# Kernel optimization log

Hardware: AMD Instinct MI355X
Metric: run time of the kernel (lower is better)

The kernel has to match this reference:

```python
import jax, jax.numpy as jnp
import numpy as np

B, L, D_MODEL, D_STATE, D_HIDDEN = 4, 4096, 1024, 256, 4096
RMIN, RMAX, MAX_PHASE = 0.8, 0.95, 2.0 * np.pi


def setup_inputs() -> dict:
    key = jax.random.key(0)
    ks = jax.random.split(key, 10)
    # LRU ring init (Orvieto et al.): |lambda| in [rmin, rmax], phase in [0, max_phase)
    u1 = jax.random.uniform(ks[0], (D_STATE,))
    u2 = jax.random.uniform(ks[1], (D_STATE,))
    nu_log = jnp.log(-0.5 * jnp.log(u1 * (RMAX**2 - RMIN**2) + RMIN**2))
    theta_log = jnp.log(MAX_PHASE * u2)
    B_re = jax.random.normal(ks[2], (D_STATE, D_MODEL)) / np.sqrt(2.0 * D_MODEL)
    B_im = jax.random.normal(ks[3], (D_STATE, D_MODEL)) / np.sqrt(2.0 * D_MODEL)
    C_re = jax.random.normal(ks[4], (D_MODEL, D_STATE)) / np.sqrt(D_STATE)
    C_im = jax.random.normal(ks[5], (D_MODEL, D_STATE)) / np.sqrt(D_STATE)
    D_mat = jax.random.normal(ks[6], (D_MODEL, D_MODEL)) / np.sqrt(D_MODEL)
    W1 = jax.random.normal(ks[7], (D_MODEL, D_HIDDEN)) * np.sqrt(2.0 / D_MODEL)
    W2 = jax.random.normal(ks[8], (D_HIDDEN, D_MODEL)) * np.sqrt(2.0 / D_HIDDEN)
    res_logit = jnp.asarray(-1.0, dtype=jnp.float32)
    x3d = jax.random.normal(ks[9], (B, L, D_MODEL), dtype=jnp.float32)
    return {"x3d": x3d, "nu_log": nu_log, "theta_log": theta_log,
            "B_re": B_re, "B_im": B_im, "C_re": C_re, "C_im": C_im,
            "D_mat": D_mat, "W1": W1, "W2": W2, "res_logit": res_logit}


def _lru_scan(lam, Bu):
    # diagonal linear recurrence x_t = lam * x_{t-1} + Bu_t via associative scan
    lam_b = jnp.broadcast_to(lam, Bu.shape)  # [B, L, N]

    def comb(a, b):
        return (a[0] * b[0], b[0] * a[1] + b[1])

    _, states = jax.lax.associative_scan(comb, (lam_b, Bu), axis=1)
    return states  # [B, L, N] complex


def reference(x3d, nu_log, theta_log, B_re, B_im, C_re, C_im, D_mat, W1, W2, res_logit):
    lam = jnp.exp(-jnp.exp(nu_log) + 1j * jnp.exp(theta_log))          # [N]
    gamma = jnp.sqrt(1.0 - jnp.abs(lam) ** 2)                           # [N]
    Bn = (gamma[:, None] * (B_re + 1j * B_im))                          # [N, D]
    Bu = jnp.einsum('bld,nd->bln', x3d.astype(jnp.complex64), Bn)       # [B, L, N]
    states = _lru_scan(lam.astype(jnp.complex64), Bu)                   # [B, L, N]
    y = jnp.einsum('bln,mn->blm', states, C_re + 1j * C_im).real \
        + jnp.einsum('bld,md->blm', x3d, D_mat)                         # [B, L, D]
    # MLP feedforward (nl_layers=2, bias=False), dropout is identity at p=0
    z = jax.nn.gelu(y @ W1) @ W2                                        # [B, L, D]
    out = x3d + jax.nn.sigmoid(res_logit) * z
    st = states[:, -1]  # final recurrent state
    return out, st
```

## Files before the change

kernel.cpp:

```cpp
#include <hip/hip_runtime.h>
#include <stdint.h>

typedef __bf16 bf16;
typedef bf16 bf16x8 __attribute__((ext_vector_type(8)));
typedef float f32x4 __attribute__((ext_vector_type(4)));

#define B_  4
#define L_  4096
#define DM  1024
#define DS  256
#define DH  4096
#define BL  16384
#define CL  64
#define NC  64

__device__ __forceinline__ float bfbits(uint32_t lo16) {
  union { uint32_t u; float f; } v; v.u = lo16 << 16; return v.f;
}

__device__ __forceinline__ void async16(const bf16* g, bf16* l) {
  __builtin_amdgcn_global_load_lds(
      (const __attribute__((address_space(1))) uint32_t*)g,
      (__attribute__((address_space(3))) uint32_t*)l, 16, 0, 0);
}

#define MEMFENCE() asm volatile("" ::: "memory")

__global__ void phaseA(const float* __restrict__ nu_log,
                       const float* __restrict__ th_log,
                       float* __restrict__ scal) {
  int n = threadIdx.x;
  float nu = __expf(nu_log[n]);
  float th = __expf(th_log[n]);
  float mod = __expf(-nu);
  float lr = mod * cosf(th);
  float li = mod * sinf(th);
  float g = sqrtf(fmaxf(1.0f - mod * mod, 0.0f));
  float pr = 1.f, pi = 0.f;
  for (int i = 0; i < CL; i++) {
    float nr = pr * lr - pi * li;
    float ni = pr * li + pi * lr;
    pr = nr; pi = ni;
  }
  scal[n] = lr; scal[256 + n] = li;
  scal[512 + n] = pr; scal[768 + n] = pi;
  scal[1024 + n] = g;
}

__global__ void prep_bu(const float* __restrict__ B_re, const float* __restrict__ B_im,
                        const float* __restrict__ scal, bf16* __restrict__ WB) {
  size_t i = (size_t)blockIdx.x * 256 + threadIdx.x;
  int row = (int)(i >> 10), col = (int)(i & 1023);
  int n = row >> 1;
  const float* src = (row & 1) ? B_im : B_re;
  WB[i] = (bf16)(scal[1024 + n] * src[n * 1024 + col]);
}

__global__ void prep_y(const float* __restrict__ C_re, const float* __restrict__ C_im,
                       const float* __restrict__ D_mat, bf16* __restrict__ WB) {
  size_t i = (size_t)blockIdx.x * 256 + threadIdx.x;
  int m = (int)(i / 1536), c = (int)(i % 1536);
  float v;
  if (c < 256)       v = C_re[m * 256 + c];
  else if (c < 512)  v = -C_im[m * 256 + (c - 256)];
  else               v = D_mat[m * 1024 + (c - 512)];
  WB[i] = (bf16)v;
}

__global__ void transpose_to_bf16(const float* __restrict__ in, bf16* __restrict__ out,
                                  int R, int C) {
  __shared__ float tile[32][33];
  int c0 = blockIdx.x * 32, r0 = blockIdx.y * 32;
  int tx = threadIdx.x, ty = threadIdx.y;
  for (int i = 0; i < 32; i += 8)
    tile[ty + i][tx] = in[(size_t)(r0 + ty + i) * C + c0 + tx];
  __syncthreads();
  for (int i = 0; i < 32; i += 8)
    out[(size_t)(c0 + ty + i) * R + r0 + tx] = (bf16)tile[tx][ty + i];
}

__global__ void conv_x(const float4* __restrict__ x, bf16* __restrict__ XS) {
  size_t i = (size_t)blockIdx.x * 256 + threadIdx.x;
  size_t t = i >> 8;
  int d4 = (int)(i & 255);
  float4 v = x[i];
  bf16* o = XS + t * 1536 + 512 + (size_t)d4 * 4;
  o[0] = (bf16)v.x; o[1] = (bf16)v.y; o[2] = (bf16)v.z; o[3] = (bf16)v.w;
}

template <int EPI>
__device__ __forceinline__ void epi_store(void* C, int ldc, size_t row, size_t col,
                                          float v, float sig, const float* xres) {
  size_t off = row * (size_t)ldc + col;
  if (EPI == 0) {
    ((bf16*)C)[off] = (bf16)v;
  } else if (EPI == 1) {
    float z = 0.7978845608f * (v + 0.044715f * v * v * v);
    float gv = v / (1.f + __expf(-2.f * z));
    ((bf16*)C)[off] = (bf16)gv;
  } else {
    ((float*)C)[off] = xres[off] + sig * v;
  }
}

template <int EPI>
__global__ __launch_bounds__(512, 2) void gemm256(
    const bf16* __restrict__ A, int lda,
    const bf16* __restrict__ Bt, int ldb,
    void* __restrict__ C, int ldc, int NK, int mt, int nt,
    const float* __restrict__ xres, const float* __restrict__ reslog) {
  __shared__ __align__(16) bf16 sA[2 * 16384];
  __shared__ __align__(16) bf16 sB[2 * 16384];

  const int tid  = threadIdx.x;
  const int lane = tid & 63;
  const int wave = tid >> 6;
  const int q = lane >> 4, l16 = lane & 15;
  const int wr = wave >> 2, wc = wave & 3;

  int nb = mt * nt;
  int per = nb >> 3;
  int t0 = (blockIdx.x & 7) * per + (blockIdx.x >> 3);
  int gsz = nt << 3;
  int g = t0 / gsz, r = t0 % gsz;
  size_t m0 = (size_t)(g * 8 + (r & 7)) * 256;
  size_t n0 = (size_t)(r >> 3) * 256;

  const int srow = tid >> 3;
  const int scol = (((tid & 7) ^ ((tid >> 3) & 7)) << 3);
  const bf16* gA = A  + (m0 + srow) * (size_t)lda + scol;
  const bf16* gB = Bt + (n0 + srow) * (size_t)ldb + scol;
  bf16* lA = sA + tid * 8;
  bf16* lB = sB + tid * 8;

  auto stageA = [&](int kt) {
    const bf16* s = gA + kt * 64;
    bf16* l = lA + (kt & 1) * 16384;
    async16(s, l);
    async16(s + (size_t)64  * lda, l + 4096);
    async16(s + (size_t)128 * lda, l + 8192);
    async16(s + (size_t)192 * lda, l + 12288);
  };
  auto stageB = [&](int kt) {
    const bf16* s = gB + kt * 64;
    bf16* l = lB + (kt & 1) * 16384;
    async16(s, l);
    async16(s + (size_t)64  * ldb, l + 4096);
    async16(s + (size_t)128 * ldb, l + 8192);
    async16(s + (size_t)192 * ldb, l + 12288);
  };

  stageA(0); stageB(0);
  __builtin_amdgcn_s_waitcnt(0x0F70);
  __builtin_amdgcn_s_barrier();
  MEMFENCE();

  const int sw  = (l16 & 7) << 3;
  const int qx0 = (q << 3) ^ sw;
  const int qx1 = ((q << 3) + 32) ^ sw;
  const bf16* Ard = sA + wr * 8192 + l16 * 64;
  const bf16* Brd = sB + (wc >> 1) * 8192 + ((wc & 1) * 64 + l16) * 64;

  f32x4 acc[8][4] = {};
  bf16x8 aL[4][2], aH[4][2], b[4][2];

  for (int t = 0; t < NK; ++t) {
    const int d = (t & 1) * 16384;
    const bf16* Ab = Ard + d;
    const bf16* Bb = Brd + d;

#pragma unroll
    for (int j = 0; j < 4; ++j) {
      aL[j][0] = *(const bf16x8*)&Ab[j * 1024 + qx0];
      aL[j][1] = *(const bf16x8*)&Ab[j * 1024 + qx1];
    }
#pragma unroll
    for (int n = 0; n < 4; ++n) {
      b[n][0] = *(const bf16x8*)&Bb[n * 1024 + qx0];
      b[n][1] = *(const bf16x8*)&Bb[n * 1024 + qx1];
    }
    if (t + 1 < NK) { stageA(t + 1); stageB(t + 1); }
    MEMFENCE();

    __builtin_amdgcn_s_setprio(1);
#pragma unroll
    for (int j = 0; j < 4; ++j)
#pragma unroll
      for (int n = 0; n < 4; ++n)
        acc[j][n] = __builtin_amdgcn_mfma_f32_16x16x32_bf16(aL[j][0], b[n][0], acc[j][n], 0, 0, 0);
#pragma unroll
    for (int j = 0; j < 4; ++j)
#pragma unroll
      for (int n = 0; n < 4; ++n)
        acc[j][n] = __builtin_amdgcn_mfma_f32_16x16x32_bf16(aL[j][1], b[n][1], acc[j][n], 0, 0, 0);

#pragma unroll
    for (int j = 0; j < 4; ++j) {
      aH[j][0] = *(const bf16x8*)&Ab[(4 + j) * 1024 + qx0];
      aH[j][1] = *(const bf16x8*)&Ab[(4 + j) * 1024 + qx1];
    }
#pragma unroll
    for (int j = 0; j < 4; ++j)
#pragma unroll
      for (int n = 0; n < 4; ++n)
        acc[4 + j][n] = __builtin_amdgcn_mfma_f32_16x16x32_bf16(aH[j][0], b[n][0], acc[4 + j][n], 0, 0, 0);
#pragma unroll
    for (int j = 0; j < 4; ++j)
#pragma unroll
      for (int n = 0; n < 4; ++n)
        acc[4 + j][n] = __builtin_amdgcn_mfma_f32_16x16x32_bf16(aH[j][1], b[n][1], acc[4 + j][n], 0, 0, 0);
    __builtin_amdgcn_s_setprio(0);

    MEMFENCE();
    __builtin_amdgcn_s_waitcnt(0x0F70);
    __builtin_amdgcn_s_barrier();
    MEMFENCE();
  }

  float sig = 0.f;
  if (EPI == 2) sig = 1.f / (1.f + __expf(-reslog[0]));
#pragma unroll
  for (int mi = 0; mi < 8; ++mi)
#pragma unroll
    for (int ni = 0; ni < 4; ++ni) {
      size_t col = n0 + wc * 64 + ni * 16 + l16;
#pragma unroll
      for (int r2 = 0; r2 < 4; ++r2) {
        size_t row = m0 + wr * 128 + mi * 16 + q * 4 + r2;
        epi_store<EPI>(C, ldc, row, col, acc[mi][ni][r2], sig, xres);
      }
    }
}

template <int EPI>
__global__ __launch_bounds__(512, 2) void gemm128(
    const bf16* __restrict__ A, int lda,
    const bf16* __restrict__ Bt, int ldb,
    void* __restrict__ C, int ldc, int NK, int mt, int nt,
    const float* __restrict__ xres, const float* __restrict__ reslog) {
  __shared__ __align__(16) bf16 sA[2 * 8192];
  __shared__ __align__(16) bf16 sB[2 * 16384];

  const int tid  = threadIdx.x;
  const int lane = tid & 63;
  const int wave = tid >> 6;
  const int q = lane >> 4, l16 = lane & 15;
  const int wr = wave >> 2, wc = wave & 3;

  int nb = mt * nt;
  int per = nb >> 3;
  int t0 = (blockIdx.x & 7) * per + (blockIdx.x >> 3);
  int gsz = nt << 3;
  int g = t0 / gsz, r = t0 % gsz;
  size_t m0 = (size_t)(g * 8 + (r & 7)) * 128;
  size_t n0 = (size_t)(r >> 3) * 256;

  const int srow = tid >> 3;
  const int scol = (((tid & 7) ^ ((tid >> 3) & 7)) << 3);
  const bf16* gA = A  + (m0 + srow) * (size_t)lda + scol;
  const bf16* gB = Bt + (n0 + srow) * (size_t)ldb + scol;
  bf16* lA = sA + tid * 8;
  bf16* lB = sB + tid * 8;

  auto stageA = [&](int kt) {
    const bf16* s = gA + kt * 64;
    bf16* l = lA + (kt & 1) * 8192;
    async16(s, l);
    async16(s + (size_t)64 * lda, l + 4096);
  };
  auto stageB = [&](int kt) {
    const bf16* s = gB + kt * 64;
    bf16* l = lB + (kt & 1) * 16384;
    async16(s, l);
    async16(s + (size_t)64  * ldb, l + 4096);
    async16(s + (size_t)128 * ldb, l + 8192);
    async16(s + (size_t)192 * ldb, l + 12288);
  };

  stageA(0); stageB(0);
  __builtin_amdgcn_s_waitcnt(0x0F70);
  __builtin_amdgcn_s_barrier();
  MEMFENCE();

  const int sw  = (l16 & 7) << 3;
  const int qx0 = (q << 3) ^ sw;
  const int qx1 = ((q << 3) + 32) ^ sw;
  const bf16* Ard = sA + (wr * 64 + l16) * 64;
  const bf16* Brd = sB + (wc >> 1) * 8192 + ((wc & 1) * 64 + l16) * 64;

  f32x4 acc[4][4] = {};
  bf16x8 a[4][2], b[4][2];

  for (int t = 0; t < NK; ++t) {
    const bf16* Ab = Ard + (t & 1) * 8192;
    const bf16* Bb = Brd + (t & 1) * 16384;

#pragma unroll
    for (int j = 0; j < 4; ++j) {
      a[j][0] = *(const bf16x8*)&Ab[j * 1024 + qx0];
      a[j][1] = *(const bf16x8*)&Ab[j * 1024 + qx1];
    }
#pragma unroll
    for (int n = 0; n < 4; ++n) {
      b[n][0] = *(const bf16x8*)&Bb[n * 1024 + qx0];
      b[n][1] = *(const bf16x8*)&Bb[n * 1024 + qx1];
    }
    if (t + 1 < NK) { stageA(t + 1); stageB(t + 1); }
    MEMFENCE();

    __builtin_amdgcn_s_setprio(1);
#pragma unroll
    for (int j = 0; j < 4; ++j)
#pragma unroll
      for (int n = 0; n < 4; ++n)
        acc[j][n] = __builtin_amdgcn_mfma_f32_16x16x32_bf16(a[j][0], b[n][0], acc[j][n], 0, 0, 0);
#pragma unroll
    for (int j = 0; j < 4; ++j)
#pragma unroll
      for (int n = 0; n < 4; ++n)
        acc[j][n] = __builtin_amdgcn_mfma_f32_16x16x32_bf16(a[j][1], b[n][1], acc[j][n], 0, 0, 0);
    __builtin_amdgcn_s_setprio(0);

    MEMFENCE();
    __builtin_amdgcn_s_waitcnt(0x0F70);
    __builtin_amdgcn_s_barrier();
    MEMFENCE();
  }

  float sig = 0.f;
  if (EPI == 2) sig = 1.f / (1.f + __expf(-reslog[0]));
#pragma unroll
  for (int mi = 0; mi < 4; ++mi)
#pragma unroll
    for (int ni = 0; ni < 4; ++ni) {
      size_t col = n0 + wc * 64 + ni * 16 + l16;
#pragma unroll
      for (int r2 = 0; r2 < 4; ++r2) {
        size_t row = m0 + wr * 64 + mi * 16 + q * 4 + r2;
        epi_store<EPI>(C, ldc, row, col, acc[mi][ni][r2], sig, xres);
      }
    }
}

__global__ void scan_pass1(const bf16* __restrict__ Bu, const float* __restrict__ scal,
                           float2* __restrict__ H) {
  int b = blockIdx.x >> 6, c = blockIdx.x & 63, n = threadIdx.x;
  float lr = scal[n], li = scal[256 + n];
  float sr = 0.f, si = 0.f;
  size_t t0 = (size_t)b * L_ + (size_t)c * CL;
  const uint32_t* p = (const uint32_t*)(Bu + t0 * 512) + n;
  for (int j = 0; j < CL; j++) {
    uint32_t u = p[(size_t)j * 256];
    float ur = bfbits(u & 0xffffu), ui = bfbits(u >> 16);
    float nr = lr * sr - li * si + ur;
    float ni = lr * si + li * sr + ui;
    sr = nr; si = ni;
  }
  H[(size_t)(b * NC + c) * 256 + n] = make_float2(sr, si);
}

__global__ void scan_pass2(const float2* __restrict__ H, const float* __restrict__ scal,
                           float2* __restrict__ Carry) {
  int b = blockIdx.x, n = threadIdx.x;
  float Pr = scal[512 + n], Pi = scal[768 + n];
  float cr = 0.f, ci = 0.f;
  for (int c = 0; c < NC; c++) {
    Carry[(size_t)(b * NC + c) * 256 + n] = make_float2(cr, ci);
    float2 h = H[(size_t)(b * NC + c) * 256 + n];
    float nr = Pr * cr - Pi * ci + h.x;
    float ni = Pr * ci + Pi * cr + h.y;
    cr = nr; ci = ni;
  }
}

__global__ void scan_pass3(const bf16* __restrict__ Bu, const float* __restrict__ scal,
                           const float2* __restrict__ Carry, bf16* __restrict__ XS,
                           float* __restrict__ st) {
  int b = blockIdx.x >> 6, c = blockIdx.x & 63, n = threadIdx.x;
  float lr = scal[n], li = scal[256 + n];
  float2 cv = Carry[(size_t)(b * NC + c) * 256 + n];
  float sr = cv.x, si = cv.y;
  size_t t0 = (size_t)b * L_ + (size_t)c * CL;
  const uint32_t* p = (const uint32_t*)(Bu + t0 * 512) + n;
  bf16* qp = XS + t0 * 1536 + n;
  for (int j = 0; j < CL; j++) {
    uint32_t u = p[(size_t)j * 256];
    float ur = bfbits(u & 0xffffu), ui = bfbits(u >> 16);
    float nr = lr * sr - li * si + ur;
    float ni = lr * si + li * sr + ui;
    sr = nr; si = ni;
    qp[(size_t)j * 1536] = (bf16)sr;
    qp[(size_t)j * 1536 + 256] = (bf16)si;
  }
  if (c == NC - 1) {
    st[(size_t)b * 256 + n] = sr;
    st[1024 + (size_t)b * 256 + n] = si;
  }
}

extern "C" void kernel_launch(void* const* d_in, const int* in_sizes, int n_in,
                              void* d_out, int out_size, void* d_ws, size_t ws_size,
                              hipStream_t stream) {
  const float* x      = (const float*)d_in[0];
  const float* nu_log = (const float*)d_in[1];
  const float* th_log = (const float*)d_in[2];
  const float* B_re   = (const float*)d_in[3];
  const float* B_im   = (const float*)d_in[4];
  const float* C_re   = (const float*)d_in[5];
  const float* C_im   = (const float*)d_in[6];
  const float* D_mat  = (const float*)d_in[7];
  const float* W1     = (const float*)d_in[8];
  const float* W2     = (const float*)d_in[9];
  const float* reslog = (const float*)d_in[10];

  char* wsb = (char*)d_ws;
  size_t off = 0;
  auto alloc = [&](size_t bytes) {
    void* p = wsb + off;
    off += (bytes + 255) & ~(size_t)255;
    return p;
  };
  float*  scal = (float*)alloc(5 * 256 * 4);
  bf16*   WBbu = (bf16*)alloc((size_t)512 * 1024 * 2);
  bf16*   WBy  = (bf16*)alloc((size_t)1024 * 1536 * 2);
  bf16*   WB1  = (bf16*)alloc((size_t)4096 * 1024 * 2);
  bf16*   WB2  = (bf16*)alloc((size_t)1024 * 4096 * 2);
  float2* H    = (float2*)alloc((size_t)B_ * NC * 256 * 8);
  float2* Cr   = (float2*)alloc((size_t)B_ * NC * 256 * 8);
  bf16*   Ybf  = (bf16*)alloc((size_t)BL * 1024 * 2);
  bf16*   XS   = (bf16*)alloc((size_t)BL * 1536 * 2);
  bf16*   Bu   = (bf16*)alloc((size_t)BL * 512 * 2);
  bf16*   Hbf  = XS;

  float* out = (float*)d_out;
  float* st  = out + (size_t)BL * DM;

  phaseA<<<1, 256, 0, stream>>>(nu_log, th_log, scal);
  prep_bu<<<512 * 1024 / 256, 256, 0, stream>>>(B_re, B_im, scal, WBbu);
  prep_y<<<1024 * 1536 / 256, 256, 0, stream>>>(C_re, C_im, D_mat, WBy);
  transpose_to_bf16<<<dim3(4096 / 32, 1024 / 32), dim3(32, 8), 0, stream>>>(W1, WB1, 1024, 4096);
  transpose_to_bf16<<<dim3(1024 / 32, 4096 / 32), dim3(32, 8), 0, stream>>>(W2, WB2, 4096, 1024);
  conv_x<<<BL * 256 / 256, 256, 0, stream>>>((const float4*)x, XS);

  gemm128<0><<<128 * 2, 512, 0, stream>>>(
      XS + 512, 1536, WBbu, 1024, Bu, 512, 16, 128, 2, nullptr, nullptr);

  scan_pass1<<<B_ * NC, 256, 0, stream>>>(Bu, scal, H);
  scan_pass2<<<B_, 256, 0, stream>>>(H, scal, Cr);
  scan_pass3<<<B_ * NC, 256, 0, stream>>>(Bu, scal, Cr, XS, st);

  gemm256<0><<<64 * 4, 512, 0, stream>>>(
      XS, 1536, WBy, 1536, Ybf, 1024, 24, 64, 4, nullptr, nullptr);

  for (int i = 0; i < 2; i++) {
    const bf16* Yc = Ybf + (size_t)i * 8192 * 1024;
    float* Oc = out + (size_t)i * 8192 * 1024;
    const float* Xc = x + (size_t)i * 8192 * 1024;
    gemm256<1><<<32 * 16, 512, 0, stream>>>(
        Yc, 1024, WB1, 1024, Hbf, 4096, 16, 32, 16, nullptr, nullptr);
    gemm128<2><<<64 * 4, 512, 0, stream>>>(
        Hbf, 4096, WB2, 4096, Oc, 1024, 64, 64, 4, Xc, reslog);
  }
}
```

Before: 569.7 us.

## Software-pipeline LDS fragment loads and prefetch global tiles two stages ahead

Both bf16 GEMM kernels are restructured so global-to-LDS copies for tile kt+2 are issued right after each barrier. The LDS-to-register fragment loads are split into halves (qx0/qx1) that are double-buffered in registers and interleaved with MFMA groups, with sched_barrier fences to keep the order. The prologue stages two tiles and uses partial vmcnt waits. The aim is to hide LDS read latency and global load latency behind MFMA work. The cost is more register pressure and an extra lgkmcnt wait before each barrier.

```diff
diff --git a/kernel.cpp b/kernel.cpp
--- a/kernel.cpp
+++ b/kernel.cpp
@@ -24,7 +24,9 @@
       (__attribute__((address_space(3))) uint32_t*)l, 16, 0, 0);
 }
 
-#define MEMFENCE() asm volatile("" ::: "memory")
+#define MEMFENCE()  asm volatile("" ::: "memory")
+#define LGKM0()     asm volatile("s_waitcnt lgkmcnt(0)" ::: "memory")
+#define SCHEDB()    __builtin_amdgcn_sched_barrier(0)
 
 __global__ void phaseA(const float* __restrict__ nu_log,
                        const float* __restrict__ th_log,
@@ -150,8 +152,8 @@
     async16(s + (size_t)192 * ldb, l + 12288);
   };
 
-  stageA(0); stageB(0);
-  __builtin_amdgcn_s_waitcnt(0x0F70);
+  stageA(0); stageB(0); stageA(1); stageB(1);
+  __builtin_amdgcn_s_waitcnt(0x0F78);
   __builtin_amdgcn_s_barrier();
   MEMFENCE();
 
@@ -162,59 +164,75 @@
   const bf16* Brd = sB + (wc >> 1) * 8192 + ((wc & 1) * 64 + l16) * 64;
 
   f32x4 acc[8][4] = {};
-  bf16x8 aL[4][2], aH[4][2], b[4][2];
-
-  for (int t = 0; t < NK; ++t) {
-    const int d = (t & 1) * 16384;
-    const bf16* Ab = Ard + d;
-    const bf16* Bb = Brd + d;
-
-#pragma unroll
-    for (int j = 0; j < 4; ++j) {
-      aL[j][0] = *(const bf16x8*)&Ab[j * 1024 + qx0];
-      aL[j][1] = *(const bf16x8*)&Ab[j * 1024 + qx1];
-    }
-#pragma unroll
-    for (int n = 0; n < 4; ++n) {
-      b[n][0] = *(const bf16x8*)&Bb[n * 1024 + qx0];
-      b[n][1] = *(const bf16x8*)&Bb[n * 1024 + qx1];
-    }
-    if (t + 1 < NK) { stageA(t + 1); stageB(t + 1); }
-    MEMFENCE();
-
-    __builtin_amdgcn_s_setprio(1);
-#pragma unroll
-    for (int j = 0; j < 4; ++j)
-#pragma unroll
-      for (int n = 0; n < 4; ++n)
-        acc[j][n] = __builtin_amdgcn_mfma_f32_16x16x32_bf16(aL[j][0], b[n][0], acc[j][n], 0, 0, 0);
-#pragma unroll
-    for (int j = 0; j < 4; ++j)
-#pragma unroll
-      for (int n = 0; n < 4; ++n)
-        acc[j][n] = __builtin_amdgcn_mfma_f32_16x16x32_bf16(aL[j][1], b[n][1], acc[j][n], 0, 0, 0);
-
-#pragma unroll
-    for (int j = 0; j < 4; ++j) {
-      aH[j][0] = *(const bf16x8*)&Ab[(4 + j) * 1024 + qx0];
-      aH[j][1] = *(const bf16x8*)&Ab[(4 + j) * 1024 + qx1];
-    }
-#pragma unroll
-    for (int j = 0; j < 4; ++j)
-#pragma unroll
-      for (int n = 0; n < 4; ++n)
-        acc[4 + j][n] = __builtin_amdgcn_mfma_f32_16x16x32_bf16(aH[j][0], b[n][0], acc[4 + j][n], 0, 0, 0);
-#pragma unroll
-    for (int j = 0; j < 4; ++j)
-#pragma unroll
-      for (int n = 0; n < 4; ++n)
-        acc[4 + j][n] = __builtin_amdgcn_mfma_f32_16x16x32_bf16(aH[j][1], b[n][1], acc[4 + j][n], 0, 0, 0);
+  bf16x8 a0[4], a1[4], b0[4], b1[4];
+
+#pragma unroll
+  for (int j = 0; j < 4; ++j) a0[j] = *(const bf16x8*)&Ard[j * 1024 + qx0];
+#pragma unroll
+  for (int n = 0; n < 4; ++n) b0[n] = *(const bf16x8*)&Brd[n * 1024 + qx0];
+
+  for (int kt = 0; kt < NK; ++kt) {
+    const bf16* Ab  = Ard + (kt & 1) * 16384;
+    const bf16* Bb  = Brd + (kt & 1) * 16384;
+    const bf16* Abn = Ard + ((kt + 1) & 1) * 16384;
+    const bf16* Bbn = Brd + ((kt + 1) & 1) * 16384;
+
+#pragma unroll
+    for (int j = 0; j < 4; ++j) a1[j] = *(const bf16x8*)&Ab[j * 1024 + qx1];
+#pragma unroll
+    for (int n = 0; n < 4; ++n) b1[n] = *(const bf16x8*)&Bb[n * 1024 + qx1];
+    SCHEDB();
+    __builtin_amdgcn_s_setprio(1);
+#pragma unroll
+    for (int j = 0; j < 4; ++j)
+#pragma unroll
+      for (int n = 0; n < 4; ++n)
+        acc[j][n] = __builtin_amdgcn_mfma_f32_16x16x32_bf16(a0[j], b0[n], acc[j][n], 0, 0, 0);
+    __builtin_amdgcn_s_setprio(0);
+
+#pragma unroll
+    for (int j = 0; j < 4; ++j) a0[j] = *(const bf16x8*)&Ab[(4 + j) * 1024 + qx0];
+    SCHEDB();
+    __builtin_amdgcn_s_setprio(1);
+#pragma unroll
+    for (int j = 0; j < 4; ++j)
+#pragma unroll
+      for (int n = 0; n < 4; ++n)
+        acc[j][n] = __builtin_amdgcn_mfma_f32_16x16x32_bf16(a1[j], b1[n], acc[j][n], 0, 0, 0);
+    __builtin_amdgcn_s_setprio(0);
+
+#pragma unroll
+    for (int j = 0; j < 4; ++j) a1[j] = *(const bf16x8*)&Ab[(4 + j) * 1024 + qx1];
+    SCHEDB();
+    __builtin_amdgcn_s_setprio(1);
+#pragma unroll
+    for (int j = 0; j < 4; ++j)
+#pragma unroll
+      for (int n = 0; n < 4; ++n)
+        acc[4 + j][n] = __builtin_amdgcn_mfma_f32_16x16x32_bf16(a0[j], b0[n], acc[4 + j][n], 0, 0, 0);
     __builtin_amdgcn_s_setprio(0);
 
     MEMFENCE();
     __builtin_amdgcn_s_waitcnt(0x0F70);
+    LGKM0();
     __builtin_amdgcn_s_barrier();
     MEMFENCE();
+
+    if (kt + 1 < NK) {
+#pragma unroll
+      for (int j = 0; j < 4; ++j) a0[j] = *(const bf16x8*)&Abn[j * 1024 + qx0];
+#pragma unroll
+      for (int n = 0; n < 4; ++n) b0[n] = *(const bf16x8*)&Bbn[n * 1024 + qx0];
+    }
+    if (kt + 2 < NK) { stageA(kt + 2); stageB(kt + 2); }
+    SCHEDB();
+    __builtin_amdgcn_s_setprio(1);
+#pragma unroll
+    for (int j = 0; j < 4; ++j)
+#pragma unroll
+      for (int n = 0; n < 4; ++n)
+        acc[4 + j][n] = __builtin_amdgcn_mfma_f32_16x16x32_bf16(a1[j], b1[n], acc[4 + j][n], 0, 0, 0);
+    __builtin_amdgcn_s_setprio(0);
   }
 
   float sig = 0.f;
@@ -277,8 +295,8 @@
     async16(s + (size_t)192 * ldb, l + 12288);
   };
 
-  stageA(0); stageB(0);
-  __builtin_amdgcn_s_waitcnt(0x0F70);
+  stageA(0); stageB(0); stageA(1); stageB(1);
+  __builtin_amdgcn_s_waitcnt(0x0F76);
   __builtin_amdgcn_s_barrier();
   MEMFENCE();
 
@@ -289,42 +307,53 @@
   const bf16* Brd = sB + (wc >> 1) * 8192 + ((wc & 1) * 64 + l16) * 64;
 
   f32x4 acc[4][4] = {};
-  bf16x8 a[4][2], b[4][2];
-
-  for (int t = 0; t < NK; ++t) {
-    const bf16* Ab = Ard + (t & 1) * 8192;
-    const bf16* Bb = Brd + (t & 1) * 16384;
-
-#pragma unroll
-    for (int j = 0; j < 4; ++j) {
-      a[j][0] = *(const bf16x8*)&Ab[j * 1024 + qx0];
-      a[j][1] = *(const bf16x8*)&Ab[j * 1024 + qx1];
-    }
-#pragma unroll
-    for (int n = 0; n < 4; ++n) {
-      b[n][0] = *(const bf16x8*)&Bb[n * 1024 + qx0];
-      b[n][1] = *(const bf16x8*)&Bb[n * 1024 + qx1];
-    }
-    if (t + 1 < NK) { stageA(t + 1); stageB(t + 1); }
-    MEMFENCE();
-
-    __builtin_amdgcn_s_setprio(1);
-#pragma unroll
-    for (int j = 0; j < 4; ++j)
-#pragma unroll
-      for (int n = 0; n < 4; ++n)
-        acc[j][n] = __builtin_amdgcn_mfma_f32_16x16x32_bf16(a[j][0], b[n][0], acc[j][n], 0, 0, 0);
-#pragma unroll
-    for (int j = 0; j < 4; ++j)
-#pragma unroll
-      for (int n = 0; n < 4; ++n)
-        acc[j][n] = __builtin_amdgcn_mfma_f32_16x16x32_bf16(a[j][1], b[n][1], acc[j][n], 0, 0, 0);
+  bf16x8 a0[4], a1[4], b0[4], b1[4];
+
+#pragma unroll
+  for (int j = 0; j < 4; ++j) a0[j] = *(const bf16x8*)&Ard[j * 1024 + qx0];
+#pragma unroll
+  for (int n = 0; n < 4; ++n) b0[n] = *(const bf16x8*)&Brd[n * 1024 + qx0];
+
+  for (int kt = 0; kt < NK; ++kt) {
+    const bf16* Ab  = Ard + (kt & 1) * 8192;
+    const bf16* Bb  = Brd + (kt & 1) * 16384;
+    const bf16* Abn = Ard + ((kt + 1) & 1) * 8192;
+    const bf16* Bbn = Brd + ((kt + 1) & 1) * 16384;
+
+#pragma unroll
+    for (int j = 0; j < 4; ++j) a1[j] = *(const bf16x8*)&Ab[j * 1024 + qx1];
+#pragma unroll
+    for (int n = 0; n < 4; ++n) b1[n] = *(const bf16x8*)&Bb[n * 1024 + qx1];
+    SCHEDB();
+    __builtin_amdgcn_s_setprio(1);
+#pragma unroll
+    for (int j = 0; j < 4; ++j)
+#pragma unroll
+      for (int n = 0; n < 4; ++n)
+        acc[j][n] = __builtin_amdgcn_mfma_f32_16x16x32_bf16(a0[j], b0[n], acc[j][n], 0, 0, 0);
     __builtin_amdgcn_s_setprio(0);
 
     MEMFENCE();
     __builtin_amdgcn_s_waitcnt(0x0F70);
+    LGKM0();
     __builtin_amdgcn_s_barrier();
     MEMFENCE();
+
+    if (kt + 1 < NK) {
+#pragma unroll
+      for (int j = 0; j < 4; ++j) a0[j] = *(const bf16x8*)&Abn[j * 1024 + qx0];
+#pragma unroll
+      for (int n = 0; n < 4; ++n) b0[n] = *(const bf16x8*)&Bbn[n * 1024 + qx0];
+    }
+    if (kt + 2 < NK) { stageA(kt + 2); stageB(kt + 2); }
+    SCHEDB();
+    __builtin_amdgcn_s_setprio(1);
+#pragma unroll
+    for (int j = 0; j < 4; ++j)
+#pragma unroll
+      for (int n = 0; n < 4; ++n)
+        acc[j][n] = __builtin_amdgcn_mfma_f32_16x16x32_bf16(a1[j], b1[n], acc[j][n], 0, 0, 0);
+    __builtin_amdgcn_s_setprio(0);
   }
 
   float sig = 0.f;
```

Result: faster. 555.9 us (-2.4%).
